# Kernel tuning notes

Hardware: AMD Instinct MI355X
Metric: run time of the kernel (lower is better)

## Reference

```python
import jax, jax.numpy as jnp
import numpy as np

B, S, I, H = 32, 512, 512, 512


def _lstm_dir(x_seq, Wih, Whh, bih, bhh, reverse):
    """Run a PyTorch-style LSTMCell over time. x_seq: [S, B, I]."""
    bsz = x_seq.shape[1]
    hid = Whh.shape[1]
    h0 = jnp.zeros((bsz, hid), x_seq.dtype)
    c0 = jnp.zeros((bsz, hid), x_seq.dtype)
    b = bih + bhh

    def step(carry, x_t):
        h, c = carry
        g = x_t @ Wih.T + h @ Whh.T + b           # [B, 4H]
        i_g, f_g, g_g, o_g = jnp.split(g, 4, axis=-1)
        c = jax.nn.sigmoid(f_g) * c + jax.nn.sigmoid(i_g) * jnp.tanh(g_g)
        h = jax.nn.sigmoid(o_g) * jnp.tanh(c)
        return (h, c), h

    (hN, cN), hs = jax.lax.scan(step, (h0, c0), x_seq, reverse=reverse)
    # with reverse=True, hs[t] is aligned with x_seq[t] (matches ht_b[::-1])
    return hs, hN, cN


def setup_inputs() -> dict:
    key = jax.random.key(0)
    ks = jax.random.split(key, 9)
    bound = 1.0 / np.sqrt(H)
    u = lambda k, shp: jax.random.uniform(k, shp, jnp.float32, -bound, bound)
    return {
        "X": jax.random.normal(ks[0], (B, S, I), jnp.float32),
        "Wih_f": u(ks[1], (4 * H, I)),
        "Whh_f": u(ks[2], (4 * H, H)),
        "bih_f": u(ks[3], (4 * H,)),
        "bhh_f": u(ks[4], (4 * H,)),
        "Wih_b": u(ks[5], (4 * H, I)),
        "Whh_b": u(ks[6], (4 * H, H)),
        "bih_b": u(ks[7], (4 * H,)),
        "bhh_b": u(ks[8], (4 * H,)),
    }


def reference(X, Wih_f, Whh_f, bih_f, bhh_f, Wih_b, Whh_b, bih_b, bhh_b):
    x_seq = jnp.transpose(X, (1, 0, 2))  # [S, B, I]
    hs_f, hN_f, cN_f = _lstm_dir(x_seq, Wih_f, Whh_f, bih_f, bhh_f, False)
    hs_b, hN_b, cN_b = _lstm_dir(x_seq, Wih_b, Whh_b, bih_b, bhh_b, True)
    # ht: [B, S, 2H]
    ht = jnp.transpose(jnp.concatenate([hs_f, hs_b], axis=-1), (1, 0, 2))
    stacked_h = jnp.stack([hN_f, hN_b])  # [2, B, H] (forward final, backward final)
    stacked_c = jnp.stack([cN_f, cN_b])
    return ht, (stacked_h, stacked_c)
```

## Files before the change

kernel.cpp:

```cpp
#include <hip/hip_runtime.h>
#include <hip/hip_bf16.h>

#define BSZ 32
#define SSZ 512
#define ISZ 512
#define HSZ 512
#define PW  32
#define XB_OFF   0ull
#define HEX_OFF  (16ull << 20)
#define CTR_OFF  (HEX_OFF + (128ull << 10))

typedef __attribute__((ext_vector_type(8)))  short short8;
typedef __attribute__((ext_vector_type(4)))  float f32x4;
typedef __attribute__((ext_vector_type(4)))  unsigned short us4;
typedef __attribute__((ext_vector_type(4)))  int i32x4;

__device__ __forceinline__ unsigned short f2bf(float f) {
    union { float f; unsigned u; } v; v.f = f;
    unsigned r = v.u + 0x7fffu + ((v.u >> 16) & 1u);
    return (unsigned short)(r >> 16);
}

__device__ __forceinline__ float sigf(float x) { return 1.0f / (1.0f + __expf(-x)); }
__device__ __forceinline__ float tanhfast(float x) {
    float a = fabsf(x);
    float e = __expf(-2.0f * a);
    float t = (1.0f - e) / (1.0f + e);
    return x < 0.0f ? -t : t;
}

__global__ void k_xpose(const float* __restrict__ X, unsigned short* __restrict__ Xb) {
    int idx = blockIdx.x * 256 + threadIdx.x;
    int i4 = idx & 127;
    int t  = (idx >> 7) & 511;
    int b  = idx >> 16;
    float4 v = reinterpret_cast<const float4*>(X)[idx];
    us4 o = { f2bf(v.x), f2bf(v.y), f2bf(v.z), f2bf(v.w) };
    *reinterpret_cast<us4*>(Xb + (size_t)t * 16384 + (size_t)(i4 >> 1) * 256 + b * 8 + (i4 & 1) * 4) = o;
}

__launch_bounds__(256, 1)
__global__ void k_bilstm(const float* __restrict__ Wih_f, const float* __restrict__ Whh_f,
                         const float* __restrict__ bih_f, const float* __restrict__ bhh_f,
                         const float* __restrict__ Wih_b, const float* __restrict__ Whh_b,
                         const float* __restrict__ bih_b, const float* __restrict__ bhh_b,
                         const unsigned short* __restrict__ Xb,
                         unsigned short* h_ex, unsigned* flags, float* __restrict__ out)
{
    const int tid = threadIdx.x;
    const int grp = blockIdx.x & 7;
    if (grp >= 2) return;
    const int dir = grp;
    const int p   = blockIdx.x >> 3;
    const int wv  = tid >> 6;
    const int ln  = tid & 63;
    const int kh  = wv >> 1;
    const int nt  = wv & 1;
    const int q   = ln >> 4;
    const int m15 = ln & 15;

    unsigned* tab = flags + 4096;
    {
        unsigned xcc;
        asm volatile("s_getreg_b32 %0, hwreg(20, 0, 32)" : "=s"(xcc));
        if (tid == 0)
            __hip_atomic_store(tab + dir * 32 + p, (xcc & 7u) + 1u,
                               __ATOMIC_RELAXED, __HIP_MEMORY_SCOPE_AGENT);
    }

    const float* Wsel = kh ? (dir ? Whh_b : Whh_f) : (dir ? Wih_b : Wih_f);
    const float* bi   = dir ? bih_b : bih_f;
    const float* bh   = dir ? bhh_b : bhh_f;

    __shared__ float gates[2][32][67];
    __shared__ float cst[32][16];
    __shared__ float bias[64];
    __shared__ int   mode_sh;

    short8 breg[16][2];
    {
        const float* wr0 = Wsel + (size_t)((nt * 2 + 0) * 512 + p * 16 + m15) * 512 + q * 8;
        const float* wr1 = Wsel + (size_t)((nt * 2 + 1) * 512 + p * 16 + m15) * 512 + q * 8;
#pragma unroll
        for (int ks = 0; ks < 16; ++ks) {
            short8 b0, b1;
#pragma unroll
            for (int j = 0; j < 8; ++j) {
                b0[j] = (short)f2bf(wr0[ks * 32 + j]);
                b1[j] = (short)f2bf(wr1[ks * 32 + j]);
            }
            breg[ks][0] = b0; breg[ks][1] = b1;
        }
    }

    if (tid < 64) {
        int c = tid;
        int gr = (c >> 4) * 512 + p * 16 + (c & 15);
        bias[c] = bi[gr] + bh[gr];
    }
    for (int i = tid; i < 512; i += 256) ((float*)cst)[i] = 0.0f;

    if (tid < 64) {
        const unsigned* tp = tab + dir * 32 + (tid & 31);
        unsigned v;
        do { v = __hip_atomic_load(tp, __ATOMIC_RELAXED, __HIP_MEMORY_SCOPE_AGENT); } while (v == 0u);
        unsigned ref = __shfl(v, 0);
        int same = (__ballot(v == ref) == ~0ull) ? 1 : 0;
        if (tid == 0) mode_sh = same;
    }
    __syncthreads();
    const int fast = mode_sh;

    unsigned* flg = flags + (size_t)dir * 2048;
    unsigned short* hexd = h_ex + (size_t)dir * 2 * 16384;

    int agent_poll = 0;

    for (int s = 0; s < 512; ++s) {
        const int t = dir ? (511 - s) : s;

        f32x4 acc00 = {0.f,0.f,0.f,0.f}, acc01 = {0.f,0.f,0.f,0.f};
        f32x4 acc10 = {0.f,0.f,0.f,0.f}, acc11 = {0.f,0.f,0.f,0.f};

        if (kh == 0) {
            const unsigned short* abase = Xb + (size_t)t * 16384;
#pragma unroll
            for (int ks = 0; ks < 16; ++ks) {
                const unsigned short* ap = abase + (size_t)(ks * 4 + q) * 256 + m15 * 8;
                short8 a0 = *reinterpret_cast<const short8*>(ap);
                short8 a1 = *reinterpret_cast<const short8*>(ap + 128);
                acc00 = __builtin_amdgcn_mfma_f32_16x16x32_bf16(a0, breg[ks][0], acc00, 0, 0, 0);
                acc01 = __builtin_amdgcn_mfma_f32_16x16x32_bf16(a0, breg[ks][1], acc01, 0, 0, 0);
                acc10 = __builtin_amdgcn_mfma_f32_16x16x32_bf16(a1, breg[ks][0], acc10, 0, 0, 0);
                acc11 = __builtin_amdgcn_mfma_f32_16x16x32_bf16(a1, breg[ks][1], acc11, 0, 0, 0);
            }
        } else if (fast) {
            if (s > 0) {
                const unsigned* fp = flg + (ln & 31);
                if (!agent_poll) {
                    int spins = 0;
                    for (;;) {
                        unsigned v;
                        asm volatile("global_load_dword %0, %1, off sc0\n\t"
                                     "s_waitcnt vmcnt(0)"
                                     : "=&v"(v) : "v"(fp) : "memory");
                        if (__ballot((int)(v >= (unsigned)s)) == ~0ull) break;
                        if (++spins > 20000) { agent_poll = 1; break; }
                    }
                }
                if (agent_poll) {
                    for (;;) {
                        unsigned v = __hip_atomic_load(fp, __ATOMIC_RELAXED, __HIP_MEMORY_SCOPE_AGENT);
                        if (__ballot((int)(v >= (unsigned)s)) == ~0ull) break;
                    }
                }
                asm volatile("" ::: "memory");
            }
            const unsigned short* abase = hexd + (size_t)((s + 1) & 1) * 16384;
            i32x4 A0[16], A1[16];
#pragma unroll
            for (int ks = 0; ks < 16; ++ks) {
                const unsigned short* ap = abase + (size_t)(ks * 4 + q) * 256 + m15 * 8;
                asm volatile("global_load_dwordx4 %0, %2, off sc0\n\t"
                             "global_load_dwordx4 %1, %3, off sc0"
                             : "=&v"(A0[ks]), "=&v"(A1[ks])
                             : "v"(ap), "v"(ap + 128) : "memory");
            }
#pragma unroll
            for (int ks = 0; ks < 16; ++ks) {
                asm volatile("s_waitcnt vmcnt(%0)" :: "n"(30 - 2 * ks) : "memory");
                __builtin_amdgcn_sched_barrier(0);
                short8 a0 = __builtin_bit_cast(short8, A0[ks]);
                short8 a1 = __builtin_bit_cast(short8, A1[ks]);
                acc00 = __builtin_amdgcn_mfma_f32_16x16x32_bf16(a0, breg[ks][0], acc00, 0, 0, 0);
                acc01 = __builtin_amdgcn_mfma_f32_16x16x32_bf16(a0, breg[ks][1], acc01, 0, 0, 0);
                acc10 = __builtin_amdgcn_mfma_f32_16x16x32_bf16(a1, breg[ks][0], acc10, 0, 0, 0);
                acc11 = __builtin_amdgcn_mfma_f32_16x16x32_bf16(a1, breg[ks][1], acc11, 0, 0, 0);
            }
        } else {
            if (s > 0) {
                const unsigned* fp = flg + (ln & 31);
                for (;;) {
                    unsigned v = __hip_atomic_load(fp, __ATOMIC_RELAXED, __HIP_MEMORY_SCOPE_AGENT);
                    if (__ballot((int)(v >= (unsigned)s)) == ~0ull) break;
                }
                asm volatile("" ::: "memory");
            }
            const unsigned* abase = reinterpret_cast<const unsigned*>(hexd + (size_t)((s + 1) & 1) * 16384);
#pragma unroll
            for (int ks = 0; ks < 16; ++ks) {
                const unsigned* ap = abase + ((ks * 4 + q) * 256 + m15 * 8) / 2;
                union { short8 s8; unsigned u[4]; } ua0, ua1;
#pragma unroll
                for (int w = 0; w < 4; ++w) {
                    ua0.u[w] = __hip_atomic_load(ap + w,      __ATOMIC_RELAXED, __HIP_MEMORY_SCOPE_AGENT);
                    ua1.u[w] = __hip_atomic_load(ap + 64 + w, __ATOMIC_RELAXED, __HIP_MEMORY_SCOPE_AGENT);
                }
                acc00 = __builtin_amdgcn_mfma_f32_16x16x32_bf16(ua0.s8, breg[ks][0], acc00, 0, 0, 0);
                acc01 = __builtin_amdgcn_mfma_f32_16x16x32_bf16(ua0.s8, breg[ks][1], acc01, 0, 0, 0);
                acc10 = __builtin_amdgcn_mfma_f32_16x16x32_bf16(ua1.s8, breg[ks][0], acc10, 0, 0, 0);
                acc11 = __builtin_amdgcn_mfma_f32_16x16x32_bf16(ua1.s8, breg[ks][1], acc11, 0, 0, 0);
            }
        }

        {
            int rb = q * 4;
            int cb = nt * 32 + m15;
#pragma unroll
            for (int r = 0; r < 4; ++r) {
                gates[kh][rb + r][cb]           = acc00[r];
                gates[kh][rb + r][cb + 16]      = acc01[r];
                gates[kh][16 + rb + r][cb]      = acc10[r];
                gates[kh][16 + rb + r][cb + 16] = acc11[r];
            }
        }
        __syncthreads();

        int b  = tid >> 3;
        int j0 = (tid & 7) * 2;
        float hv01[2], cn01[2];
        {
#pragma unroll
            for (int u = 0; u < 2; ++u) {
                int j = j0 + u;
                float ig = gates[0][b][j]      + gates[1][b][j]      + bias[j];
                float fg = gates[0][b][16 + j] + gates[1][b][16 + j] + bias[16 + j];
                float gg = gates[0][b][32 + j] + gates[1][b][32 + j] + bias[32 + j];
                float og = gates[0][b][48 + j] + gates[1][b][48 + j] + bias[48 + j];
                float cn = sigf(fg) * cst[b][j] + sigf(ig) * tanhfast(gg);
                cst[b][j] = cn;
                float hv = sigf(og) * tanhfast(cn);
                hv01[u] = hv; cn01[u] = cn;
            }
            int hc0 = p * 16 + j0;
            unsigned pk = (unsigned)f2bf(hv01[0]) | ((unsigned)f2bf(hv01[1]) << 16);
            unsigned* dst = reinterpret_cast<unsigned*>(
                hexd + (size_t)(s & 1) * 16384 + (size_t)(hc0 >> 3) * 256 + b * 8 + (hc0 & 7));
            if (fast) {
                asm volatile("global_store_dword %0, %1, off sc0" :: "v"(dst), "v"(pk) : "memory");
            } else {
                __hip_atomic_store(dst, pk, __ATOMIC_RELAXED, __HIP_MEMORY_SCOPE_AGENT);
            }
        }

        asm volatile("s_waitcnt vmcnt(0)" ::: "memory");
        __syncthreads();
        if (tid == 0) {
            if (fast) {
                unsigned sv = (unsigned)(s + 1);
                asm volatile("global_store_dword %0, %1, off sc0" :: "v"(flg + p), "v"(sv) : "memory");
            } else {
                __hip_atomic_store(flg + p, (unsigned)(s + 1), __ATOMIC_RELAXED, __HIP_MEMORY_SCOPE_AGENT);
            }
        }

#pragma unroll
        for (int u = 0; u < 2; ++u) {
            int hc = p * 16 + j0 + u;
            out[(size_t)b * (512 * 1024) + (size_t)t * 1024 + dir * 512 + hc] = hv01[u];
            if (s == 511) {
                out[16777216 + dir * 16384 + b * 512 + hc] = hv01[u];
                out[16777216 + 32768 + dir * 16384 + b * 512 + hc] = cn01[u];
            }
        }
    }
}

extern "C" void kernel_launch(void* const* d_in, const int* in_sizes, int n_in,
                              void* d_out, int out_size, void* d_ws, size_t ws_size,
                              hipStream_t stream) {
    const float* X     = (const float*)d_in[0];
    const float* Wih_f = (const float*)d_in[1];
    const float* Whh_f = (const float*)d_in[2];
    const float* bih_f = (const float*)d_in[3];
    const float* bhh_f = (const float*)d_in[4];
    const float* Wih_b = (const float*)d_in[5];
    const float* Whh_b = (const float*)d_in[6];
    const float* bih_b = (const float*)d_in[7];
    const float* bhh_b = (const float*)d_in[8];
    float* out = (float*)d_out;

    unsigned short* Xb   = (unsigned short*)((char*)d_ws + XB_OFF);
    unsigned short* h_ex = (unsigned short*)((char*)d_ws + HEX_OFF);
    unsigned*       flg  = (unsigned*)((char*)d_ws + CTR_OFF);

    hipMemsetAsync((char*)d_ws + HEX_OFF, 0, (128ull + 64ull) << 10, stream);
    k_xpose<<<8192, 256, 0, stream>>>(X, Xb);
    k_bilstm<<<256, 256, 0, stream>>>(Wih_f, Whh_f, bih_f, bhh_f,
                                      Wih_b, Whh_b, bih_b, bhh_b,
                                      Xb, h_ex, flg, out);
}
```

Baseline: 2.562 ms.

## Split K across waves, prefetch X into LDS via DMA, defer output stores

Each wave now owns all four gate groups over half of the K dimension instead of two gate groups over the full K. Partial sums from four waves are combined in shared memory. The x-input tile for the next timestep is prefetched into double-buffered LDS with global_load_lds, so the input projection no longer waits on global loads. Hidden-state outputs are staged in LDS and written one step later as vectorized float4 stores by the input waves, keeping them off the recurrent critical path. The cost is more LDS traffic, a four-way gate reduction, and more intricate vmcnt bookkeeping.

After: 2.998 ms. 1.17x slower.

```diff
diff --git a/kernel.cpp b/kernel.cpp
--- a/kernel.cpp
+++ b/kernel.cpp
@@ -27,6 +27,11 @@
     float e = __expf(-2.0f * a);
     float t = (1.0f - e) / (1.0f + e);
     return x < 0.0f ? -t : t;
+}
+
+__device__ __forceinline__ void dma16(const unsigned short* g, unsigned short* l) {
+    __builtin_amdgcn_global_load_lds((const __attribute__((address_space(1))) unsigned int*)(g),
+                                     (__attribute__((address_space(3))) unsigned int*)(l), 16, 0, 0);
 }
 
 __global__ void k_xpose(const float* __restrict__ X, unsigned short* __restrict__ Xb) {
@@ -50,14 +55,14 @@
     const int tid = threadIdx.x;
     const int grp = blockIdx.x & 7;
     if (grp >= 2) return;
-    const int dir = grp;
-    const int p   = blockIdx.x >> 3;
-    const int wv  = tid >> 6;
-    const int ln  = tid & 63;
-    const int kh  = wv >> 1;
-    const int nt  = wv & 1;
-    const int q   = ln >> 4;
-    const int m15 = ln & 15;
+    const int dir  = grp;
+    const int p    = blockIdx.x >> 3;
+    const int wv   = tid >> 6;
+    const int ln   = tid & 63;
+    const int kh   = wv >> 1;
+    const int half = wv & 1;
+    const int q    = ln >> 4;
+    const int m15  = ln & 15;
 
     unsigned* tab = flags + 4096;
     {
@@ -72,24 +77,24 @@
     const float* bi   = dir ? bih_b : bih_f;
     const float* bh   = dir ? bhh_b : bhh_f;
 
-    __shared__ float gates[2][32][67];
+    __shared__ float gates[4][32][67];
     __shared__ float cst[32][16];
+    __shared__ float outbuf[2][32][16];
     __shared__ float bias[64];
     __shared__ int   mode_sh;
-
-    short8 breg[16][2];
-    {
-        const float* wr0 = Wsel + (size_t)((nt * 2 + 0) * 512 + p * 16 + m15) * 512 + q * 8;
-        const float* wr1 = Wsel + (size_t)((nt * 2 + 1) * 512 + p * 16 + m15) * 512 + q * 8;
-#pragma unroll
-        for (int ks = 0; ks < 16; ++ks) {
-            short8 b0, b1;
-#pragma unroll
-            for (int j = 0; j < 8; ++j) {
-                b0[j] = (short)f2bf(wr0[ks * 32 + j]);
-                b1[j] = (short)f2bf(wr1[ks * 32 + j]);
-            }
-            breg[ks][0] = b0; breg[ks][1] = b1;
+    __shared__ __align__(16) unsigned short xstage[2][2][8192];
+
+    short8 breg[8][4];
+#pragma unroll
+    for (int ks = 0; ks < 8; ++ks) {
+#pragma unroll
+        for (int g = 0; g < 4; ++g) {
+            const float* wr = Wsel + (size_t)(g * 512 + p * 16 + m15) * 512
+                                   + half * 256 + ks * 32 + q * 8;
+            short8 bb;
+#pragma unroll
+            for (int j = 0; j < 8; ++j) bb[j] = (short)f2bf(wr[j]);
+            breg[ks][g] = bb;
         }
     }
 
@@ -114,25 +119,42 @@
     unsigned* flg = flags + (size_t)dir * 2048;
     unsigned short* hexd = h_ex + (size_t)dir * 2 * 16384;
 
+    if (kh == 0) {
+        int t0 = dir ? 511 : 0;
+        const unsigned short* src = Xb + (size_t)t0 * 16384 + half * 8192 + ln * 8;
+        unsigned short* lb = &xstage[half][0][0];
+#pragma unroll
+        for (int j = 0; j < 16; ++j) dma16(src + j * 512, lb + j * 512);
+    }
+
     int agent_poll = 0;
 
     for (int s = 0; s < 512; ++s) {
-        const int t = dir ? (511 - s) : s;
-
-        f32x4 acc00 = {0.f,0.f,0.f,0.f}, acc01 = {0.f,0.f,0.f,0.f};
-        f32x4 acc10 = {0.f,0.f,0.f,0.f}, acc11 = {0.f,0.f,0.f,0.f};
+        f32x4 acc[4][2];
+#pragma unroll
+        for (int g = 0; g < 4; ++g) { acc[g][0] = {0.f,0.f,0.f,0.f}; acc[g][1] = {0.f,0.f,0.f,0.f}; }
 
         if (kh == 0) {
-            const unsigned short* abase = Xb + (size_t)t * 16384;
-#pragma unroll
-            for (int ks = 0; ks < 16; ++ks) {
-                const unsigned short* ap = abase + (size_t)(ks * 4 + q) * 256 + m15 * 8;
+            asm volatile("s_waitcnt vmcnt(0)" ::: "memory");
+            __builtin_amdgcn_sched_barrier(0);
+            const unsigned short* xs = &xstage[half][s & 1][0];
+#pragma unroll
+            for (int ks = 0; ks < 8; ++ks) {
+                const unsigned short* ap = xs + (ks * 4 + q) * 256 + m15 * 8;
                 short8 a0 = *reinterpret_cast<const short8*>(ap);
                 short8 a1 = *reinterpret_cast<const short8*>(ap + 128);
-                acc00 = __builtin_amdgcn_mfma_f32_16x16x32_bf16(a0, breg[ks][0], acc00, 0, 0, 0);
-                acc01 = __builtin_amdgcn_mfma_f32_16x16x32_bf16(a0, breg[ks][1], acc01, 0, 0, 0);
-                acc10 = __builtin_amdgcn_mfma_f32_16x16x32_bf16(a1, breg[ks][0], acc10, 0, 0, 0);
-                acc11 = __builtin_amdgcn_mfma_f32_16x16x32_bf16(a1, breg[ks][1], acc11, 0, 0, 0);
+#pragma unroll
+                for (int g = 0; g < 4; ++g) {
+                    acc[g][0] = __builtin_amdgcn_mfma_f32_16x16x32_bf16(a0, breg[ks][g], acc[g][0], 0, 0, 0);
+                    acc[g][1] = __builtin_amdgcn_mfma_f32_16x16x32_bf16(a1, breg[ks][g], acc[g][1], 0, 0, 0);
+                }
+            }
+            if (s > 0) {
+                int pt = dir ? (512 - s) : (s - 1);
+                int L = half * 64 + ln; int b = L >> 2; int qd = L & 3;
+                f32x4 hvv = *reinterpret_cast<const f32x4*>(&outbuf[(s - 1) & 1][b][qd * 4]);
+                *reinterpret_cast<f32x4*>(&out[(size_t)b * 524288 + (size_t)pt * 1024
+                                               + dir * 512 + p * 16 + qd * 4]) = hvv;
             }
         } else if (fast) {
             if (s > 0) {
@@ -156,26 +178,27 @@
                 }
                 asm volatile("" ::: "memory");
             }
-            const unsigned short* abase = hexd + (size_t)((s + 1) & 1) * 16384;
-            i32x4 A0[16], A1[16];
-#pragma unroll
-            for (int ks = 0; ks < 16; ++ks) {
-                const unsigned short* ap = abase + (size_t)(ks * 4 + q) * 256 + m15 * 8;
+            const unsigned short* ab = hexd + (size_t)((s + 1) & 1) * 16384 + half * 8192;
+            i32x4 A0[8], A1[8];
+#pragma unroll
+            for (int ks = 0; ks < 8; ++ks) {
+                const unsigned short* ap = ab + (ks * 4 + q) * 256 + m15 * 8;
                 asm volatile("global_load_dwordx4 %0, %2, off sc0\n\t"
                              "global_load_dwordx4 %1, %3, off sc0"
                              : "=&v"(A0[ks]), "=&v"(A1[ks])
                              : "v"(ap), "v"(ap + 128) : "memory");
             }
 #pragma unroll
-            for (int ks = 0; ks < 16; ++ks) {
-                asm volatile("s_waitcnt vmcnt(%0)" :: "n"(30 - 2 * ks) : "memory");
+            for (int ks = 0; ks < 8; ++ks) {
+                asm volatile("s_waitcnt vmcnt(%0)" :: "n"(14 - 2 * ks) : "memory");
                 __builtin_amdgcn_sched_barrier(0);
                 short8 a0 = __builtin_bit_cast(short8, A0[ks]);
                 short8 a1 = __builtin_bit_cast(short8, A1[ks]);
-                acc00 = __builtin_amdgcn_mfma_f32_16x16x32_bf16(a0, breg[ks][0], acc00, 0, 0, 0);
-                acc01 = __builtin_amdgcn_mfma_f32_16x16x32_bf16(a0, breg[ks][1], acc01, 0, 0, 0);
-                acc10 = __builtin_amdgcn_mfma_f32_16x16x32_bf16(a1, breg[ks][0], acc10, 0, 0, 0);
-                acc11 = __builtin_amdgcn_mfma_f32_16x16x32_bf16(a1, breg[ks][1], acc11, 0, 0, 0);
+#pragma unroll
+                for (int g = 0; g < 4; ++g) {
+                    acc[g][0] = __builtin_amdgcn_mfma_f32_16x16x32_bf16(a0, breg[ks][g], acc[g][0], 0, 0, 0);
+                    acc[g][1] = __builtin_amdgcn_mfma_f32_16x16x32_bf16(a1, breg[ks][g], acc[g][1], 0, 0, 0);
+                }
             }
         } else {
             if (s > 0) {
@@ -188,50 +211,48 @@
             }
             const unsigned* abase = reinterpret_cast<const unsigned*>(hexd + (size_t)((s + 1) & 1) * 16384);
 #pragma unroll
-            for (int ks = 0; ks < 16; ++ks) {
-                const unsigned* ap = abase + ((ks * 4 + q) * 256 + m15 * 8) / 2;
+            for (int ks = 0; ks < 8; ++ks) {
+                const unsigned* ap = abase + ((half * 32 + ks * 4 + q) * 256 + m15 * 8) / 2;
                 union { short8 s8; unsigned u[4]; } ua0, ua1;
 #pragma unroll
                 for (int w = 0; w < 4; ++w) {
                     ua0.u[w] = __hip_atomic_load(ap + w,      __ATOMIC_RELAXED, __HIP_MEMORY_SCOPE_AGENT);
                     ua1.u[w] = __hip_atomic_load(ap + 64 + w, __ATOMIC_RELAXED, __HIP_MEMORY_SCOPE_AGENT);
                 }
-                acc00 = __builtin_amdgcn_mfma_f32_16x16x32_bf16(ua0.s8, breg[ks][0], acc00, 0, 0, 0);
-                acc01 = __builtin_amdgcn_mfma_f32_16x16x32_bf16(ua0.s8, breg[ks][1], acc01, 0, 0, 0);
-                acc10 = __builtin_amdgcn_mfma_f32_16x16x32_bf16(ua1.s8, breg[ks][0], acc10, 0, 0, 0);
-                acc11 = __builtin_amdgcn_mfma_f32_16x16x32_bf16(ua1.s8, breg[ks][1], acc11, 0, 0, 0);
-            }
-        }
+#pragma unroll
+                for (int g = 0; g < 4; ++g) {
+                    acc[g][0] = __builtin_amdgcn_mfma_f32_16x16x32_bf16(ua0.s8, breg[ks][g], acc[g][0], 0, 0, 0);
+                    acc[g][1] = __builtin_amdgcn_mfma_f32_16x16x32_bf16(ua1.s8, breg[ks][g], acc[g][1], 0, 0, 0);
+                }
+            }
+        }
+
+#pragma unroll
+        for (int g = 0; g < 4; ++g)
+#pragma unroll
+            for (int r = 0; r < 4; ++r) {
+                gates[wv][q * 4 + r][g * 16 + m15]      = acc[g][0][r];
+                gates[wv][16 + q * 4 + r][g * 16 + m15] = acc[g][1][r];
+            }
+        asm volatile("s_waitcnt lgkmcnt(0)" ::: "memory");
+        __builtin_amdgcn_s_barrier();
 
         {
-            int rb = q * 4;
-            int cb = nt * 32 + m15;
-#pragma unroll
-            for (int r = 0; r < 4; ++r) {
-                gates[kh][rb + r][cb]           = acc00[r];
-                gates[kh][rb + r][cb + 16]      = acc01[r];
-                gates[kh][16 + rb + r][cb]      = acc10[r];
-                gates[kh][16 + rb + r][cb + 16] = acc11[r];
-            }
-        }
-        __syncthreads();
-
-        int b  = tid >> 3;
-        int j0 = (tid & 7) * 2;
-        float hv01[2], cn01[2];
-        {
+            int b  = tid >> 3;
+            int j0 = (tid & 7) * 2;
+            float hv01[2];
 #pragma unroll
             for (int u = 0; u < 2; ++u) {
                 int j = j0 + u;
-                float ig = gates[0][b][j]      + gates[1][b][j]      + bias[j];
-                float fg = gates[0][b][16 + j] + gates[1][b][16 + j] + bias[16 + j];
-                float gg = gates[0][b][32 + j] + gates[1][b][32 + j] + bias[32 + j];
-                float og = gates[0][b][48 + j] + gates[1][b][48 + j] + bias[48 + j];
+                float ig = gates[0][b][j]      + gates[1][b][j]      + gates[2][b][j]      + gates[3][b][j]      + bias[j];
+                float fg = gates[0][b][16 + j] + gates[1][b][16 + j] + gates[2][b][16 + j] + gates[3][b][16 + j] + bias[16 + j];
+                float gg = gates[0][b][32 + j] + gates[1][b][32 + j] + gates[2][b][32 + j] + gates[3][b][32 + j] + bias[32 + j];
+                float og = gates[0][b][48 + j] + gates[1][b][48 + j] + gates[2][b][48 + j] + gates[3][b][48 + j] + bias[48 + j];
                 float cn = sigf(fg) * cst[b][j] + sigf(ig) * tanhfast(gg);
                 cst[b][j] = cn;
-                float hv = sigf(og) * tanhfast(cn);
-                hv01[u] = hv; cn01[u] = cn;
-            }
+                hv01[u] = sigf(og) * tanhfast(cn);
+            }
+            *reinterpret_cast<float2*>(&outbuf[s & 1][b][j0]) = make_float2(hv01[0], hv01[1]);
             int hc0 = p * 16 + j0;
             unsigned pk = (unsigned)f2bf(hv01[0]) | ((unsigned)f2bf(hv01[1]) << 16);
             unsigned* dst = reinterpret_cast<unsigned*>(
@@ -243,8 +264,22 @@
             }
         }
 
-        asm volatile("s_waitcnt vmcnt(0)" ::: "memory");
-        __syncthreads();
+        if (kh == 0 && s < 511) {
+            int tn = dir ? (510 - s) : (s + 1);
+            const unsigned short* src = Xb + (size_t)tn * 16384 + half * 8192 + ln * 8;
+            unsigned short* lb = &xstage[half][(s + 1) & 1][0];
+#pragma unroll
+            for (int j = 0; j < 16; ++j) dma16(src + j * 512, lb + j * 512);
+        }
+
+        if (kh == 0) {
+            if (s < 511) { asm volatile("s_waitcnt vmcnt(16)" ::: "memory"); }
+            else         { asm volatile("s_waitcnt vmcnt(0)"  ::: "memory"); }
+        } else {
+            asm volatile("s_waitcnt vmcnt(0)" ::: "memory");
+        }
+        asm volatile("s_waitcnt lgkmcnt(0)" ::: "memory");
+        __builtin_amdgcn_s_barrier();
         if (tid == 0) {
             if (fast) {
                 unsigned sv = (unsigned)(s + 1);
@@ -253,16 +288,17 @@
                 __hip_atomic_store(flg + p, (unsigned)(s + 1), __ATOMIC_RELAXED, __HIP_MEMORY_SCOPE_AGENT);
             }
         }
-
-#pragma unroll
-        for (int u = 0; u < 2; ++u) {
-            int hc = p * 16 + j0 + u;
-            out[(size_t)b * (512 * 1024) + (size_t)t * 1024 + dir * 512 + hc] = hv01[u];
-            if (s == 511) {
-                out[16777216 + dir * 16384 + b * 512 + hc] = hv01[u];
-                out[16777216 + 32768 + dir * 16384 + b * 512 + hc] = cn01[u];
-            }
-        }
+    }
+
+    if (kh == 0) {
+        int L = half * 64 + ln; int b = L >> 2; int qd = L & 3;
+        int tl = dir ? 0 : 511;
+        f32x4 hvv = *reinterpret_cast<const f32x4*>(&outbuf[1][b][qd * 4]);
+        *reinterpret_cast<f32x4*>(&out[(size_t)b * 524288 + (size_t)tl * 1024
+                                       + dir * 512 + p * 16 + qd * 4]) = hvv;
+        *reinterpret_cast<f32x4*>(&out[16777216 + dir * 16384 + b * 512 + p * 16 + qd * 4]) = hvv;
+        f32x4 cvv = *reinterpret_cast<const f32x4*>(&cst[b][qd * 4]);
+        *reinterpret_cast<f32x4*>(&out[16777216 + 32768 + dir * 16384 + b * 512 + p * 16 + qd * 4]) = cvv;
     }
 }
 
```

## Prefetch X tiles into LDS via async DMA and defer output stores

Applied to the files above, without the earlier changes.

The input-projection waves now prefetch the X slice for upcoming timesteps into a triple-buffered LDS stage using global_load_lds, so the recurrence no longer waits on global X loads each step. Hidden-state outputs are staged in a double-buffered LDS outbuf and written one step late as vectorized float4 stores by the kh==0 waves, taking scattered scalar stores off the critical path. The final h/c are stored after the loop. Barriers are replaced with explicit waitcnt plus s_barrier, and an s_sleep is added to the flag spin loop. This costs extra LDS and relies on careful vmcnt accounting.

Measured after the change: 3.379 ms. +31.9%, slower.

```diff
diff --git a/kernel.cpp b/kernel.cpp
--- a/kernel.cpp
+++ b/kernel.cpp
@@ -5,7 +5,6 @@
 #define SSZ 512
 #define ISZ 512
 #define HSZ 512
-#define PW  32
 #define XB_OFF   0ull
 #define HEX_OFF  (16ull << 20)
 #define CTR_OFF  (HEX_OFF + (128ull << 10))
@@ -27,6 +26,11 @@
     float e = __expf(-2.0f * a);
     float t = (1.0f - e) / (1.0f + e);
     return x < 0.0f ? -t : t;
+}
+
+__device__ __forceinline__ void dma16(const unsigned short* g, unsigned short* l) {
+    __builtin_amdgcn_global_load_lds((const __attribute__((address_space(1))) unsigned int*)(g),
+                                     (__attribute__((address_space(3))) unsigned int*)(l), 16, 0, 0);
 }
 
 __global__ void k_xpose(const float* __restrict__ X, unsigned short* __restrict__ Xb) {
@@ -74,8 +78,10 @@
 
     __shared__ float gates[2][32][67];
     __shared__ float cst[32][16];
+    __shared__ float outbuf[2][32][16];
     __shared__ float bias[64];
     __shared__ int   mode_sh;
+    __shared__ __align__(16) unsigned short xstage[3][16384];
 
     short8 breg[16][2];
     {
@@ -114,19 +120,39 @@
     unsigned* flg = flags + (size_t)dir * 2048;
     unsigned short* hexd = h_ex + (size_t)dir * 2 * 16384;
 
+    if (kh == 0) {
+#pragma unroll
+        for (int pre = 0; pre < 2; ++pre) {
+            int t0 = dir ? (511 - pre) : pre;
+            const unsigned short* src = Xb + (size_t)t0 * 16384 + nt * 8192 + ln * 8;
+            unsigned short* lb = &xstage[pre][nt * 8192];
+#pragma unroll
+            for (int j = 0; j < 16; ++j) dma16(src + j * 512, lb + j * 512);
+        }
+    }
+
     int agent_poll = 0;
+    int cur = 0;
 
     for (int s = 0; s < 512; ++s) {
-        const int t = dir ? (511 - s) : s;
-
         f32x4 acc00 = {0.f,0.f,0.f,0.f}, acc01 = {0.f,0.f,0.f,0.f};
         f32x4 acc10 = {0.f,0.f,0.f,0.f}, acc11 = {0.f,0.f,0.f,0.f};
 
         if (kh == 0) {
-            const unsigned short* abase = Xb + (size_t)t * 16384;
+            if (s > 0) {
+                int pt = dir ? (512 - s) : (s - 1);
+                int L = nt * 64 + ln; int b = L >> 2; int qd = L & 3;
+                f32x4 hvv = *reinterpret_cast<const f32x4*>(&outbuf[(s - 1) & 1][b][qd * 4]);
+                *reinterpret_cast<f32x4*>(&out[(size_t)b * 524288 + (size_t)pt * 1024
+                                               + dir * 512 + p * 16 + qd * 4]) = hvv;
+            } else {
+                asm volatile("s_waitcnt vmcnt(16)" ::: "memory");
+            }
+            __builtin_amdgcn_sched_barrier(0);
+            const unsigned short* xs = &xstage[cur][0];
 #pragma unroll
             for (int ks = 0; ks < 16; ++ks) {
-                const unsigned short* ap = abase + (size_t)(ks * 4 + q) * 256 + m15 * 8;
+                const unsigned short* ap = xs + (ks * 4 + q) * 256 + m15 * 8;
                 short8 a0 = *reinterpret_cast<const short8*>(ap);
                 short8 a1 = *reinterpret_cast<const short8*>(ap + 128);
                 acc00 = __builtin_amdgcn_mfma_f32_16x16x32_bf16(a0, breg[ks][0], acc00, 0, 0, 0);
@@ -146,6 +172,7 @@
                                      : "=&v"(v) : "v"(fp) : "memory");
                         if (__ballot((int)(v >= (unsigned)s)) == ~0ull) break;
                         if (++spins > 20000) { agent_poll = 1; break; }
+                        asm volatile("s_sleep 1" ::: "memory");
                     }
                 }
                 if (agent_poll) {
@@ -156,11 +183,11 @@
                 }
                 asm volatile("" ::: "memory");
             }
-            const unsigned short* abase = hexd + (size_t)((s + 1) & 1) * 16384;
+            const unsigned short* ab = hexd + (size_t)((s + 1) & 1) * 16384;
             i32x4 A0[16], A1[16];
 #pragma unroll
             for (int ks = 0; ks < 16; ++ks) {
-                const unsigned short* ap = abase + (size_t)(ks * 4 + q) * 256 + m15 * 8;
+                const unsigned short* ap = ab + (size_t)(ks * 4 + q) * 256 + m15 * 8;
                 asm volatile("global_load_dwordx4 %0, %2, off sc0\n\t"
                              "global_load_dwordx4 %1, %3, off sc0"
                              : "=&v"(A0[ks]), "=&v"(A1[ks])
@@ -214,12 +241,14 @@
                 gates[kh][16 + rb + r][cb + 16] = acc11[r];
             }
         }
-        __syncthreads();
-
-        int b  = tid >> 3;
-        int j0 = (tid & 7) * 2;
-        float hv01[2], cn01[2];
+        asm volatile("s_waitcnt lgkmcnt(0)" ::: "memory");
+        __builtin_amdgcn_s_barrier();
+        __builtin_amdgcn_sched_barrier(0);
+
         {
+            int b  = tid >> 3;
+            int j0 = (tid & 7) * 2;
+            float hv01[2];
 #pragma unroll
             for (int u = 0; u < 2; ++u) {
                 int j = j0 + u;
@@ -229,9 +258,9 @@
                 float og = gates[0][b][48 + j] + gates[1][b][48 + j] + bias[48 + j];
                 float cn = sigf(fg) * cst[b][j] + sigf(ig) * tanhfast(gg);
                 cst[b][j] = cn;
-                float hv = sigf(og) * tanhfast(cn);
-                hv01[u] = hv; cn01[u] = cn;
-            }
+                hv01[u] = sigf(og) * tanhfast(cn);
+            }
+            *reinterpret_cast<float2*>(&outbuf[s & 1][b][j0]) = make_float2(hv01[0], hv01[1]);
             int hc0 = p * 16 + j0;
             unsigned pk = (unsigned)f2bf(hv01[0]) | ((unsigned)f2bf(hv01[1]) << 16);
             unsigned* dst = reinterpret_cast<unsigned*>(
@@ -243,8 +272,21 @@
             }
         }
 
-        asm volatile("s_waitcnt vmcnt(0)" ::: "memory");
-        __syncthreads();
+        if (kh == 0) {
+            int nxt = cur + 2; if (nxt >= 3) nxt -= 3;
+            int sp = s + 2; int tn = sp > 511 ? 511 : sp;
+            int tx = dir ? (511 - tn) : tn;
+            const unsigned short* src = Xb + (size_t)tx * 16384 + nt * 8192 + ln * 8;
+            unsigned short* lb = &xstage[nxt][nt * 8192];
+#pragma unroll
+            for (int j = 0; j < 16; ++j) dma16(src + j * 512, lb + j * 512);
+            asm volatile("s_waitcnt vmcnt(16)" ::: "memory");
+        } else {
+            asm volatile("s_waitcnt vmcnt(0)" ::: "memory");
+        }
+        asm volatile("s_waitcnt lgkmcnt(0)" ::: "memory");
+        __builtin_amdgcn_s_barrier();
+        __builtin_amdgcn_sched_barrier(0);
         if (tid == 0) {
             if (fast) {
                 unsigned sv = (unsigned)(s + 1);
@@ -253,16 +295,18 @@
                 __hip_atomic_store(flg + p, (unsigned)(s + 1), __ATOMIC_RELAXED, __HIP_MEMORY_SCOPE_AGENT);
             }
         }
-
-#pragma unroll
-        for (int u = 0; u < 2; ++u) {
-            int hc = p * 16 + j0 + u;
-            out[(size_t)b * (512 * 1024) + (size_t)t * 1024 + dir * 512 + hc] = hv01[u];
-            if (s == 511) {
-                out[16777216 + dir * 16384 + b * 512 + hc] = hv01[u];
-                out[16777216 + 32768 + dir * 16384 + b * 512 + hc] = cn01[u];
-            }
-        }
+        cur = (cur + 1 == 3) ? 0 : cur + 1;
+    }
+
+    if (kh == 0) {
+        int L = nt * 64 + ln; int b = L >> 2; int qd = L & 3;
+        int tl = dir ? 0 : 511;
+        f32x4 hvv = *reinterpret_cast<const f32x4*>(&outbuf[1][b][qd * 4]);
+        *reinterpret_cast<f32x4*>(&out[(size_t)b * 524288 + (size_t)tl * 1024
+                                       + dir * 512 + p * 16 + qd * 4]) = hvv;
+        *reinterpret_cast<f32x4*>(&out[16777216 + dir * 16384 + b * 512 + p * 16 + qd * 4]) = hvv;
+        f32x4 cvv = *reinterpret_cast<const f32x4*>(&cst[b][qd * 4]);
+        *reinterpret_cast<f32x4*>(&out[16777216 + 32768 + dir * 16384 + b * 512 + p * 16 + qd * 4]) = cvv;
     }
 }
 
```

## Precompute input projection in a separate parallel kernel before recurrent loop

Applied to the files above, without the earlier changes.

Hoists the X·Wih^T input projection out of the sequential recurrence into a separate fully parallel kernel that writes fp32 gate pre-activations to workspace. The recurrent kernel then loads these per step, and all four waves split the K dimension of h·Whh^T instead of half the waves doing input work. This shortens the serial per-step critical path. In exchange it adds 256MB of workspace traffic and an extra launch, and falls back to the old kernel if the workspace is too small.

After: 2.555 ms. No clear change (-0.3%).

```diff
diff --git a/kernel.cpp b/kernel.cpp
--- a/kernel.cpp
+++ b/kernel.cpp
@@ -5,10 +5,11 @@
 #define SSZ 512
 #define ISZ 512
 #define HSZ 512
-#define PW  32
 #define XB_OFF   0ull
 #define HEX_OFF  (16ull << 20)
 #define CTR_OFF  (HEX_OFF + (128ull << 10))
+#define XG_OFF   (32ull << 20)
+#define WS_NEED  (XG_OFF + (256ull << 20))
 
 typedef __attribute__((ext_vector_type(8)))  short short8;
 typedef __attribute__((ext_vector_type(4)))  float f32x4;
@@ -40,12 +41,284 @@
 }
 
 __launch_bounds__(256, 1)
-__global__ void k_bilstm(const float* __restrict__ Wih_f, const float* __restrict__ Whh_f,
-                         const float* __restrict__ bih_f, const float* __restrict__ bhh_f,
-                         const float* __restrict__ Wih_b, const float* __restrict__ Whh_b,
-                         const float* __restrict__ bih_b, const float* __restrict__ bhh_b,
-                         const unsigned short* __restrict__ Xb,
-                         unsigned short* h_ex, unsigned* flags, float* __restrict__ out)
+__global__ void k_xproj(const float* __restrict__ Wih_f, const float* __restrict__ Wih_b,
+                        const unsigned short* __restrict__ Xb, float* __restrict__ xg)
+{
+    const int tid = threadIdx.x;
+    const int bid = blockIdx.x;
+    const int dir = bid & 1;
+    const int p   = (bid >> 1) & 31;
+    const int tq  = bid >> 6;
+    const int wv  = tid >> 6;
+    const int ln  = tid & 63;
+    const int q   = ln >> 4;
+    const int m15 = ln & 15;
+
+    const float* Wih = dir ? Wih_b : Wih_f;
+
+    short8 breg[16];
+#pragma unroll
+    for (int ks = 0; ks < 16; ++ks) {
+        const float* wr = Wih + (size_t)(wv * 512 + p * 16 + m15) * 512 + ks * 32 + q * 8;
+        short8 bb;
+#pragma unroll
+        for (int j = 0; j < 8; ++j) bb[j] = (short)f2bf(wr[j]);
+        breg[ks] = bb;
+    }
+
+    for (int tt = 0; tt < 128; ++tt) {
+        int t = tq * 128 + tt;
+        const unsigned short* ab = Xb + (size_t)t * 16384;
+        f32x4 acc0 = {0.f,0.f,0.f,0.f}, acc1 = {0.f,0.f,0.f,0.f};
+#pragma unroll
+        for (int ks = 0; ks < 16; ++ks) {
+            const unsigned short* ap = ab + (ks * 4 + q) * 256 + m15 * 8;
+            short8 a0 = *reinterpret_cast<const short8*>(ap);
+            short8 a1 = *reinterpret_cast<const short8*>(ap + 128);
+            acc0 = __builtin_amdgcn_mfma_f32_16x16x32_bf16(a0, breg[ks], acc0, 0, 0, 0);
+            acc1 = __builtin_amdgcn_mfma_f32_16x16x32_bf16(a1, breg[ks], acc1, 0, 0, 0);
+        }
+        float* ob = xg + (((size_t)(dir * 512 + t) * 32 + p) * 2048);
+#pragma unroll
+        for (int r = 0; r < 4; ++r) {
+            ob[(q * 4 + r) * 64      + wv * 16 + m15] = acc0[r];
+            ob[(16 + q * 4 + r) * 64 + wv * 16 + m15] = acc1[r];
+        }
+    }
+}
+
+__launch_bounds__(256, 1)
+__global__ void k_bilstm2(const float* __restrict__ Whh_f, const float* __restrict__ Whh_b,
+                          const float* __restrict__ bih_f, const float* __restrict__ bhh_f,
+                          const float* __restrict__ bih_b, const float* __restrict__ bhh_b,
+                          const float* __restrict__ xg,
+                          unsigned short* h_ex, unsigned* flags, float* __restrict__ out)
+{
+    const int tid = threadIdx.x;
+    const int grp = blockIdx.x & 7;
+    if (grp >= 2) return;
+    const int dir = grp;
+    const int p   = blockIdx.x >> 3;
+    const int wv  = tid >> 6;
+    const int ln  = tid & 63;
+    const int q   = ln >> 4;
+    const int m15 = ln & 15;
+
+    unsigned* tab = flags + 4096;
+    {
+        unsigned xcc;
+        asm volatile("s_getreg_b32 %0, hwreg(20, 0, 32)" : "=s"(xcc));
+        if (tid == 0)
+            __hip_atomic_store(tab + dir * 32 + p, (xcc & 7u) + 1u,
+                               __ATOMIC_RELAXED, __HIP_MEMORY_SCOPE_AGENT);
+    }
+
+    const float* Whh = dir ? Whh_b : Whh_f;
+    const float* bi  = dir ? bih_b : bih_f;
+    const float* bh  = dir ? bhh_b : bhh_f;
+
+    __shared__ float gates[4][32][67];
+    __shared__ float cst[32][16];
+    __shared__ float bias[64];
+    __shared__ int   mode_sh;
+
+    short8 breg[4][4];
+#pragma unroll
+    for (int ksl = 0; ksl < 4; ++ksl)
+#pragma unroll
+        for (int g = 0; g < 4; ++g) {
+            const float* wr = Whh + (size_t)(g * 512 + p * 16 + m15) * 512
+                                  + wv * 128 + ksl * 32 + q * 8;
+            short8 bb;
+#pragma unroll
+            for (int j = 0; j < 8; ++j) bb[j] = (short)f2bf(wr[j]);
+            breg[ksl][g] = bb;
+        }
+
+    if (tid < 64) {
+        int c = tid;
+        int gr = (c >> 4) * 512 + p * 16 + (c & 15);
+        bias[c] = bi[gr] + bh[gr];
+    }
+    for (int i = tid; i < 512; i += 256) ((float*)cst)[i] = 0.0f;
+
+    if (tid < 64) {
+        const unsigned* tp = tab + dir * 32 + (tid & 31);
+        unsigned v;
+        do { v = __hip_atomic_load(tp, __ATOMIC_RELAXED, __HIP_MEMORY_SCOPE_AGENT); } while (v == 0u);
+        unsigned ref = __shfl(v, 0);
+        int same = (__ballot(v == ref) == ~0ull) ? 1 : 0;
+        if (tid == 0) mode_sh = same;
+    }
+    __syncthreads();
+    const int fast = mode_sh;
+
+    unsigned* flg = flags + (size_t)dir * 2048;
+    unsigned short* hexd = h_ex + (size_t)dir * 2 * 16384;
+
+    const int b  = tid >> 3;
+    const int j0 = (tid & 7) * 2;
+
+    int agent_poll = 0;
+
+    for (int s = 0; s < 512; ++s) {
+        const int t = dir ? (511 - s) : s;
+        const float* xgp = xg + ((size_t)(dir * 512 + t) * 32 + p) * 2048 + b * 64 + j0;
+
+        f32x4 acc[4][2];
+#pragma unroll
+        for (int g = 0; g < 4; ++g) { acc[g][0] = {0.f,0.f,0.f,0.f}; acc[g][1] = {0.f,0.f,0.f,0.f}; }
+        float2 xgv[4];
+
+        if (fast) {
+            if (s > 0) {
+                const unsigned* fp = flg + wv * 8 + (ln & 7);
+                if (!agent_poll) {
+                    int spins = 0;
+                    for (;;) {
+                        unsigned v;
+                        asm volatile("global_load_dword %0, %1, off sc0\n\t"
+                                     "s_waitcnt vmcnt(0)"
+                                     : "=&v"(v) : "v"(fp) : "memory");
+                        if (__ballot((int)(v >= (unsigned)s)) == ~0ull) break;
+                        if (++spins > 20000) { agent_poll = 1; break; }
+                    }
+                }
+                if (agent_poll) {
+                    for (;;) {
+                        unsigned v = __hip_atomic_load(fp, __ATOMIC_RELAXED, __HIP_MEMORY_SCOPE_AGENT);
+                        if (__ballot((int)(v >= (unsigned)s)) == ~0ull) break;
+                    }
+                }
+                asm volatile("" ::: "memory");
+            }
+            const unsigned short* ab = hexd + (size_t)((s + 1) & 1) * 16384 + wv * 4096;
+            i32x4 A0[4], A1[4];
+#pragma unroll
+            for (int ksl = 0; ksl < 4; ++ksl) {
+                const unsigned short* ap = ab + (ksl * 4 + q) * 256 + m15 * 8;
+                asm volatile("global_load_dwordx4 %0, %2, off sc0\n\t"
+                             "global_load_dwordx4 %1, %3, off sc0"
+                             : "=&v"(A0[ksl]), "=&v"(A1[ksl])
+                             : "v"(ap), "v"(ap + 128) : "memory");
+            }
+#pragma unroll
+            for (int g = 0; g < 4; ++g)
+                asm volatile("global_load_dwordx2 %0, %1, off"
+                             : "=v"(xgv[g]) : "v"(xgp + g * 16) : "memory");
+#pragma unroll
+            for (int ksl = 0; ksl < 4; ++ksl) {
+                asm volatile("s_waitcnt vmcnt(%0)" :: "n"(10 - 2 * ksl) : "memory");
+                __builtin_amdgcn_sched_barrier(0);
+                short8 a0 = __builtin_bit_cast(short8, A0[ksl]);
+                short8 a1 = __builtin_bit_cast(short8, A1[ksl]);
+#pragma unroll
+                for (int g = 0; g < 4; ++g) {
+                    acc[g][0] = __builtin_amdgcn_mfma_f32_16x16x32_bf16(a0, breg[ksl][g], acc[g][0], 0, 0, 0);
+                    acc[g][1] = __builtin_amdgcn_mfma_f32_16x16x32_bf16(a1, breg[ksl][g], acc[g][1], 0, 0, 0);
+                }
+            }
+        } else {
+            if (s > 0) {
+                const unsigned* fp = flg + (ln & 31);
+                for (;;) {
+                    unsigned v = __hip_atomic_load(fp, __ATOMIC_RELAXED, __HIP_MEMORY_SCOPE_AGENT);
+                    if (__ballot((int)(v >= (unsigned)s)) == ~0ull) break;
+                }
+                asm volatile("" ::: "memory");
+            }
+            const unsigned* abase = reinterpret_cast<const unsigned*>(
+                hexd + (size_t)((s + 1) & 1) * 16384 + wv * 4096);
+#pragma unroll
+            for (int ksl = 0; ksl < 4; ++ksl) {
+                const unsigned* ap = abase + ((ksl * 4 + q) * 256 + m15 * 8) / 2;
+                union { short8 s8; unsigned u[4]; } ua0, ua1;
+#pragma unroll
+                for (int w = 0; w < 4; ++w) {
+                    ua0.u[w] = __hip_atomic_load(ap + w,      __ATOMIC_RELAXED, __HIP_MEMORY_SCOPE_AGENT);
+                    ua1.u[w] = __hip_atomic_load(ap + 64 + w, __ATOMIC_RELAXED, __HIP_MEMORY_SCOPE_AGENT);
+                }
+#pragma unroll
+                for (int g = 0; g < 4; ++g) {
+                    acc[g][0] = __builtin_amdgcn_mfma_f32_16x16x32_bf16(ua0.s8, breg[ksl][g], acc[g][0], 0, 0, 0);
+                    acc[g][1] = __builtin_amdgcn_mfma_f32_16x16x32_bf16(ua1.s8, breg[ksl][g], acc[g][1], 0, 0, 0);
+                }
+            }
+#pragma unroll
+            for (int g = 0; g < 4; ++g)
+                xgv[g] = *reinterpret_cast<const float2*>(xgp + g * 16);
+        }
+
+#pragma unroll
+        for (int g = 0; g < 4; ++g)
+#pragma unroll
+            for (int r = 0; r < 4; ++r) {
+                gates[wv][q * 4 + r][g * 16 + m15]      = acc[g][0][r];
+                gates[wv][16 + q * 4 + r][g * 16 + m15] = acc[g][1][r];
+            }
+        asm volatile("s_waitcnt lgkmcnt(0)" ::: "memory");
+        __builtin_amdgcn_s_barrier();
+        asm volatile("s_waitcnt vmcnt(0)" ::: "memory");
+        __builtin_amdgcn_sched_barrier(0);
+
+        {
+            float hv01[2], cn01[2];
+#pragma unroll
+            for (int u = 0; u < 2; ++u) {
+                int j = j0 + u;
+                float ig = gates[0][b][j]      + gates[1][b][j]      + gates[2][b][j]      + gates[3][b][j]
+                         + (u ? xgv[0].y : xgv[0].x) + bias[j];
+                float fg = gates[0][b][16 + j] + gates[1][b][16 + j] + gates[2][b][16 + j] + gates[3][b][16 + j]
+                         + (u ? xgv[1].y : xgv[1].x) + bias[16 + j];
+                float gg = gates[0][b][32 + j] + gates[1][b][32 + j] + gates[2][b][32 + j] + gates[3][b][32 + j]
+                         + (u ? xgv[2].y : xgv[2].x) + bias[32 + j];
+                float og = gates[0][b][48 + j] + gates[1][b][48 + j] + gates[2][b][48 + j] + gates[3][b][48 + j]
+                         + (u ? xgv[3].y : xgv[3].x) + bias[48 + j];
+                float cn = sigf(fg) * cst[b][j] + sigf(ig) * tanhfast(gg);
+                cst[b][j] = cn;
+                hv01[u] = sigf(og) * tanhfast(cn);
+                cn01[u] = cn;
+            }
+            int hc0 = p * 16 + j0;
+            unsigned pk = (unsigned)f2bf(hv01[0]) | ((unsigned)f2bf(hv01[1]) << 16);
+            unsigned* dst = reinterpret_cast<unsigned*>(
+                hexd + (size_t)(s & 1) * 16384 + (size_t)(hc0 >> 3) * 256 + b * 8 + (hc0 & 7));
+            if (fast) {
+                asm volatile("global_store_dword %0, %1, off sc0" :: "v"(dst), "v"(pk) : "memory");
+            } else {
+                __hip_atomic_store(dst, pk, __ATOMIC_RELAXED, __HIP_MEMORY_SCOPE_AGENT);
+            }
+            *reinterpret_cast<float2*>(&out[(size_t)b * 524288 + (size_t)t * 1024
+                                            + dir * 512 + hc0]) = make_float2(hv01[0], hv01[1]);
+            if (s == 511) {
+                *reinterpret_cast<float2*>(&out[16777216 + dir * 16384 + b * 512 + hc0])
+                    = make_float2(hv01[0], hv01[1]);
+                *reinterpret_cast<float2*>(&out[16777216 + 32768 + dir * 16384 + b * 512 + hc0])
+                    = make_float2(cn01[0], cn01[1]);
+            }
+        }
+
+        asm volatile("s_waitcnt vmcnt(0)" ::: "memory");
+        asm volatile("s_waitcnt lgkmcnt(0)" ::: "memory");
+        __builtin_amdgcn_s_barrier();
+        if (tid == 0) {
+            if (fast) {
+                unsigned sv = (unsigned)(s + 1);
+                asm volatile("global_store_dword %0, %1, off sc0" :: "v"(flg + p), "v"(sv) : "memory");
+            } else {
+                __hip_atomic_store(flg + p, (unsigned)(s + 1), __ATOMIC_RELAXED, __HIP_MEMORY_SCOPE_AGENT);
+            }
+        }
+    }
+}
+
+__launch_bounds__(256, 1)
+__global__ void k_bilstm_fb(const float* __restrict__ Wih_f, const float* __restrict__ Whh_f,
+                            const float* __restrict__ bih_f, const float* __restrict__ bhh_f,
+                            const float* __restrict__ Wih_b, const float* __restrict__ Whh_b,
+                            const float* __restrict__ bih_b, const float* __restrict__ bhh_b,
+                            const unsigned short* __restrict__ Xb,
+                            unsigned short* h_ex, unsigned* flags, float* __restrict__ out)
 {
     const int tid = threadIdx.x;
     const int grp = blockIdx.x & 7;
@@ -118,7 +391,6 @@
 
     for (int s = 0; s < 512; ++s) {
         const int t = dir ? (511 - s) : s;
-
         f32x4 acc00 = {0.f,0.f,0.f,0.f}, acc01 = {0.f,0.f,0.f,0.f};
         f32x4 acc10 = {0.f,0.f,0.f,0.f}, acc11 = {0.f,0.f,0.f,0.f};
 
@@ -156,11 +428,11 @@
                 }
                 asm volatile("" ::: "memory");
             }
-            const unsigned short* abase = hexd + (size_t)((s + 1) & 1) * 16384;
+            const unsigned short* ab = hexd + (size_t)((s + 1) & 1) * 16384;
             i32x4 A0[16], A1[16];
 #pragma unroll
             for (int ks = 0; ks < 16; ++ks) {
-                const unsigned short* ap = abase + (size_t)(ks * 4 + q) * 256 + m15 * 8;
+                const unsigned short* ap = ab + (size_t)(ks * 4 + q) * 256 + m15 * 8;
                 asm volatile("global_load_dwordx4 %0, %2, off sc0\n\t"
                              "global_load_dwordx4 %1, %3, off sc0"
                              : "=&v"(A0[ks]), "=&v"(A1[ks])
@@ -283,10 +555,18 @@
     unsigned short* Xb   = (unsigned short*)((char*)d_ws + XB_OFF);
     unsigned short* h_ex = (unsigned short*)((char*)d_ws + HEX_OFF);
     unsigned*       flg  = (unsigned*)((char*)d_ws + CTR_OFF);
+    float*          xg   = (float*)((char*)d_ws + XG_OFF);
 
     hipMemsetAsync((char*)d_ws + HEX_OFF, 0, (128ull + 64ull) << 10, stream);
     k_xpose<<<8192, 256, 0, stream>>>(X, Xb);
-    k_bilstm<<<256, 256, 0, stream>>>(Wih_f, Whh_f, bih_f, bhh_f,
-                                      Wih_b, Whh_b, bih_b, bhh_b,
-                                      Xb, h_ex, flg, out);
-}
+
+    if (ws_size >= WS_NEED) {
+        k_xproj<<<256, 256, 0, stream>>>(Wih_f, Wih_b, Xb, xg);
+        k_bilstm2<<<256, 256, 0, stream>>>(Whh_f, Whh_b, bih_f, bhh_f, bih_b, bhh_b,
+                                           xg, h_ex, flg, out);
+    } else {
+        k_bilstm_fb<<<256, 256, 0, stream>>>(Wih_f, Whh_f, bih_f, bhh_f,
+                                             Wih_b, Whh_b, bih_b, bhh_b,
+                                             Xb, h_ex, flg, out);
+    }
+}
```
